# Optimization experiments

Hardware: AMD Instinct MI355X
Metric: run time of the kernel (lower is better)

Reference implementation:

```python
import jax, jax.numpy as jnp
import numpy as np

SCALE = 1.0  # module scale
# dropout is treated as identity (eval mode / deterministic reference)

def setup_inputs() -> dict:
    key = jax.random.key(0)
    k_x, k_w, k1, k2, k3 = jax.random.split(key, 5)
    B, S, D = 4, 4096, 1280
    x = jax.random.normal(k_x, (B, S, D), dtype=jnp.float32)
    W = jax.random.normal(k_w, (D, D), dtype=jnp.float32) * 0.02  # linear.weight [out, in]
    # kron factors are initialized to identity in the module; perturb slightly
    # so the rotation is non-trivial for correctness testing.
    kron_1 = jnp.eye(4, dtype=jnp.float32) + 0.01 * jax.random.normal(k1, (4, 4), dtype=jnp.float32)
    kron_2 = jnp.eye(8, dtype=jnp.float32) + 0.01 * jax.random.normal(k2, (8, 8), dtype=jnp.float32)
    kron_3 = jnp.eye(40, dtype=jnp.float32) + 0.01 * jax.random.normal(k3, (40, 40), dtype=jnp.float32)
    return {"x": x, "W": W, "kron_1": kron_1, "kron_2": kron_2, "kron_3": kron_3}

def reference(x, W, kron_1, kron_2, kron_3):
    # rotate_matrix = kron(kron(k1, k2), k3)  -> [in, in] = [1280, 1280]
    R = jnp.kron(jnp.kron(kron_1, kron_2), kron_3)
    # rotated_weight = (R @ W^T)^T ; F.linear(x, rotated_weight) = x @ (R @ W^T)
    rotated_weight = (R @ W.T).T  # [out, in]
    out = jnp.einsum('bsd,od->bso', x, rotated_weight)
    return out * SCALE
```

## Files before the change

kernel.cpp:

```cpp
#include <hip/hip_runtime.h>
#include <hip/hip_bf16.h>
#include <stdint.h>

typedef __bf16 bf16x8 __attribute__((ext_vector_type(8)));
typedef float floatx4 __attribute__((ext_vector_type(4)));

__device__ __forceinline__ void async_copy16(void* lds, const void* g) {
    __builtin_amdgcn_global_load_lds(
        (const __attribute__((address_space(1))) unsigned int*)g,
        (__attribute__((address_space(3))) unsigned int*)lds,
        16, 0, 0);
}

__global__ __launch_bounds__(256)
void prep(const float* __restrict__ x,
          const float* __restrict__ W,
          const float* __restrict__ K1,
          const float* __restrict__ K2,
          const float* __restrict__ K3,
          __hip_bfloat16* __restrict__ x_bf,
          __hip_bfloat16* __restrict__ Wrot,
          int nConv) {
    const int tid = threadIdx.x;

    if ((int)blockIdx.x < nConv) {
        const size_t i = ((size_t)blockIdx.x * 256 + tid) * 8;
        const float4 a = *(const float4*)(x + i);
        const float4 b = *(const float4*)(x + i + 4);
        bf16x8 v;
        v[0] = (__bf16)a.x; v[1] = (__bf16)a.y; v[2] = (__bf16)a.z; v[3] = (__bf16)a.w;
        v[4] = (__bf16)b.x; v[5] = (__bf16)b.y; v[6] = (__bf16)b.z; v[7] = (__bf16)b.w;
        *(bf16x8*)((__bf16*)x_bf + i) = v;
        return;
    }

    const int o = blockIdx.x - nConv;
    __shared__ __align__(16) float w0[1280];
    __shared__ __align__(16) float t1[1280];
    __shared__ __align__(16) float k3s[1600];
    __shared__ float k2s[64];
    __shared__ float k1s[16];

    for (int i = tid; i < 1280; i += 256) w0[i] = W[o * 1280 + i];
    for (int i = tid; i < 1600; i += 256) k3s[i] = K3[i];
    if (tid < 64) k2s[tid] = K2[tid];
    if (tid < 16) k1s[tid] = K1[tid];
    __syncthreads();

    for (int i = tid; i < 1280; i += 256) {
        const int p = i / 40, d3 = i % 40;
        const float4* w4 = (const float4*)(w0 + p * 40);
        const float4* k4 = (const float4*)(k3s + d3 * 40);
        float acc = 0.f;
#pragma unroll
        for (int t = 0; t < 10; ++t) {
            const float4 a = w4[t], b = k4[t];
            acc += a.x * b.x + a.y * b.y + a.z * b.z + a.w * b.w;
        }
        t1[i] = acc;
    }
    __syncthreads();

    for (int i = tid; i < 1280; i += 256) {
        const int d3 = i % 40, pd = i / 40;
        const int k1 = pd >> 3, d2 = pd & 7;
        float acc = 0.f;
#pragma unroll
        for (int k2 = 0; k2 < 8; ++k2) acc += t1[(k1 * 8 + k2) * 40 + d3] * k2s[d2 * 8 + k2];
        w0[i] = acc;
    }
    __syncthreads();

    for (int i = tid; i < 1280; i += 256) {
        const int d3 = i % 40, pd = i / 40;
        const int d1 = pd >> 3, d2 = pd & 7;
        float acc = 0.f;
#pragma unroll
        for (int k1 = 0; k1 < 4; ++k1) acc += w0[(k1 * 8 + d2) * 40 + d3] * k1s[d1 * 4 + k1];
        Wrot[(size_t)o * 1280 + i] = __float2bfloat16(acc);
    }
}

#define BM 128
#define BN 128
#define BK 64

__global__ __launch_bounds__(256)
void gemm_bt(const __hip_bfloat16* __restrict__ A,
             const __hip_bfloat16* __restrict__ B,
             float* __restrict__ C,
             int M, int N, int K) {
    __shared__ bf16x8 As[1024];
    __shared__ bf16x8 Bs[1024];

    const int tid  = threadIdx.x;
    const int wave = tid >> 6;
    const int lane = tid & 63;
    const int q    = lane >> 4;
    const int r16  = lane & 15;

    const int nTilesN = N / BN;
    const int bn = blockIdx.x % nTilesN;
    const int bm = blockIdx.x / nTilesN;
    const int tileM = bm * BM, tileN = bn * BN;
    const int wm = wave >> 1, wn = wave & 1;

    floatx4 acc[4][4];
#pragma unroll
    for (int i = 0; i < 4; ++i)
#pragma unroll
        for (int j = 0; j < 4; ++j) acc[i][j] = (floatx4){0.f, 0.f, 0.f, 0.f};

    for (int kt = 0; kt < K; kt += BK) {
#pragma unroll
        for (int t = 0; t < 4; ++t) {
            const int g  = wave * 256 + t * 64 + lane;
            const int m  = g >> 3;
            const int sl = g & 7;
            const int kv = sl ^ (m & 7);
            async_copy16(&As[wave * 256 + t * 64],
                         A + (size_t)(tileM + m) * K + kt + kv * 8);
            async_copy16(&Bs[wave * 256 + t * 64],
                         B + (size_t)(tileN + m) * K + kt + kv * 8);
        }
        __syncthreads();

#pragma unroll
        for (int s = 0; s < 2; ++s) {
            bf16x8 af[4], bfr[4];
            const int kv = s * 4 + q;
#pragma unroll
            for (int i = 0; i < 4; ++i) {
                const int m = wm * 64 + i * 16 + r16;
                af[i] = As[m * 8 + (kv ^ (m & 7))];
                const int n = wn * 64 + i * 16 + r16;
                bfr[i] = Bs[n * 8 + (kv ^ (n & 7))];
            }
#pragma unroll
            for (int i = 0; i < 4; ++i)
#pragma unroll
                for (int j = 0; j < 4; ++j)
                    acc[i][j] = __builtin_amdgcn_mfma_f32_16x16x32_bf16(
                        af[i], bfr[j], acc[i][j], 0, 0, 0);
        }
        __syncthreads();
    }

#pragma unroll
    for (int i = 0; i < 4; ++i) {
#pragma unroll
        for (int j = 0; j < 4; ++j) {
            const int col = tileN + wn * 64 + j * 16 + r16;
#pragma unroll
            for (int r = 0; r < 4; ++r) {
                const int row = tileM + wm * 64 + i * 16 + q * 4 + r;
                C[(size_t)row * N + col] = acc[i][j][r];
            }
        }
    }
}

extern "C" void kernel_launch(void* const* d_in, const int* in_sizes, int n_in,
                              void* d_out, int out_size, void* d_ws, size_t ws_size,
                              hipStream_t stream) {
    const float* x  = (const float*)d_in[0];
    const float* W  = (const float*)d_in[1];
    const float* K1 = (const float*)d_in[2];
    const float* K2 = (const float*)d_in[3];
    const float* K3 = (const float*)d_in[4];
    float* out = (float*)d_out;

    const int D = 1280;
    const int M = in_sizes[0] / D;
    const int N = D, K = D;

    __hip_bfloat16* x_bf = (__hip_bfloat16*)d_ws;
    __hip_bfloat16* Wrot = x_bf + (size_t)M * K;

    const int nConv = (M * K) / (256 * 8);
    prep<<<nConv + D, 256, 0, stream>>>(x, W, K1, K2, K3, x_bf, Wrot, nConv);
    gemm_bt<<<(M / BM) * (N / BN), 256, 0, stream>>>(x_bf, Wrot, out, M, N, K);
}
```

Measured before the change: 251.4 us.

## Fuse fp32-to-bf16 conversion of x into GEMM A-tile loading with register prefetch

Removes the separate pass that converted x to bf16 in workspace. The GEMM now loads fp32 A tiles directly into registers, converts them to bf16 and stores them into swizzled LDS. The next tile is prefetched into registers while MFMAs run, and the loop's trailing barrier moves to the start of the next iteration. This saves a full write and read of the bf16 activation copy, but each block now reads fp32 A, doubling the bytes per redundant tile read across column blocks and adding register pressure.

```diff
diff --git a/kernel.cpp b/kernel.cpp
--- a/kernel.cpp
+++ b/kernel.cpp
@@ -13,33 +13,18 @@
 }
 
 __global__ __launch_bounds__(256)
-void prep(const float* __restrict__ x,
-          const float* __restrict__ W,
-          const float* __restrict__ K1,
-          const float* __restrict__ K2,
-          const float* __restrict__ K3,
-          __hip_bfloat16* __restrict__ x_bf,
-          __hip_bfloat16* __restrict__ Wrot,
-          int nConv) {
-    const int tid = threadIdx.x;
-
-    if ((int)blockIdx.x < nConv) {
-        const size_t i = ((size_t)blockIdx.x * 256 + tid) * 8;
-        const float4 a = *(const float4*)(x + i);
-        const float4 b = *(const float4*)(x + i + 4);
-        bf16x8 v;
-        v[0] = (__bf16)a.x; v[1] = (__bf16)a.y; v[2] = (__bf16)a.z; v[3] = (__bf16)a.w;
-        v[4] = (__bf16)b.x; v[5] = (__bf16)b.y; v[6] = (__bf16)b.z; v[7] = (__bf16)b.w;
-        *(bf16x8*)((__bf16*)x_bf + i) = v;
-        return;
-    }
-
-    const int o = blockIdx.x - nConv;
+void kron_rotate_w(const float* __restrict__ W,
+                   const float* __restrict__ K1,
+                   const float* __restrict__ K2,
+                   const float* __restrict__ K3,
+                   __hip_bfloat16* __restrict__ Wrot) {
     __shared__ __align__(16) float w0[1280];
     __shared__ __align__(16) float t1[1280];
     __shared__ __align__(16) float k3s[1600];
     __shared__ float k2s[64];
     __shared__ float k1s[16];
+    const int o   = blockIdx.x;
+    const int tid = threadIdx.x;
 
     for (int i = tid; i < 1280; i += 256) w0[i] = W[o * 1280 + i];
     for (int i = tid; i < 1600; i += 256) k3s[i] = K3[i];
@@ -86,7 +71,7 @@
 #define BK 64
 
 __global__ __launch_bounds__(256)
-void gemm_bt(const __hip_bfloat16* __restrict__ A,
+void gemm_bt(const float* __restrict__ A,
              const __hip_bfloat16* __restrict__ B,
              float* __restrict__ C,
              int M, int N, int K) {
@@ -111,19 +96,52 @@
 #pragma unroll
         for (int j = 0; j < 4; ++j) acc[i][j] = (floatx4){0.f, 0.f, 0.f, 0.f};
 
+    int amrow[4], akv[4];
+#pragma unroll
+    for (int t = 0; t < 4; ++t) {
+        const int g = wave * 256 + t * 64 + lane;
+        amrow[t] = g >> 3;
+        akv[t]   = (g & 7) ^ (amrow[t] & 7);
+    }
+
+    float4 apre[4][2];
+#pragma unroll
+    for (int t = 0; t < 4; ++t) {
+        const float* ga = A + (size_t)(tileM + amrow[t]) * K + akv[t] * 8;
+        apre[t][0] = *(const float4*)ga;
+        apre[t][1] = *(const float4*)(ga + 4);
+    }
+
     for (int kt = 0; kt < K; kt += BK) {
+        __syncthreads();
+
+#pragma unroll
+        for (int t = 0; t < 4; ++t) {
+            bf16x8 v;
+            v[0] = (__bf16)apre[t][0].x; v[1] = (__bf16)apre[t][0].y;
+            v[2] = (__bf16)apre[t][0].z; v[3] = (__bf16)apre[t][0].w;
+            v[4] = (__bf16)apre[t][1].x; v[5] = (__bf16)apre[t][1].y;
+            v[6] = (__bf16)apre[t][1].z; v[7] = (__bf16)apre[t][1].w;
+            As[wave * 256 + t * 64 + lane] = v;
+        }
 #pragma unroll
         for (int t = 0; t < 4; ++t) {
             const int g  = wave * 256 + t * 64 + lane;
             const int m  = g >> 3;
-            const int sl = g & 7;
-            const int kv = sl ^ (m & 7);
-            async_copy16(&As[wave * 256 + t * 64],
-                         A + (size_t)(tileM + m) * K + kt + kv * 8);
+            const int kv = (g & 7) ^ (m & 7);
             async_copy16(&Bs[wave * 256 + t * 64],
                          B + (size_t)(tileN + m) * K + kt + kv * 8);
         }
         __syncthreads();
+
+        if (kt + BK < K) {
+#pragma unroll
+            for (int t = 0; t < 4; ++t) {
+                const float* ga = A + (size_t)(tileM + amrow[t]) * K + (kt + BK) + akv[t] * 8;
+                apre[t][0] = *(const float4*)ga;
+                apre[t][1] = *(const float4*)(ga + 4);
+            }
+        }
 
 #pragma unroll
         for (int s = 0; s < 2; ++s) {
@@ -143,7 +161,6 @@
                     acc[i][j] = __builtin_amdgcn_mfma_f32_16x16x32_bf16(
                         af[i], bfr[j], acc[i][j], 0, 0, 0);
         }
-        __syncthreads();
     }
 
 #pragma unroll
@@ -174,10 +191,8 @@
     const int M = in_sizes[0] / D;
     const int N = D, K = D;
 
-    __hip_bfloat16* x_bf = (__hip_bfloat16*)d_ws;
-    __hip_bfloat16* Wrot = x_bf + (size_t)M * K;
+    __hip_bfloat16* Wrot = (__hip_bfloat16*)d_ws;
 
-    const int nConv = (M * K) / (256 * 8);
-    prep<<<nConv + D, 256, 0, stream>>>(x, W, K1, K2, K3, x_bf, Wrot, nConv);
-    gemm_bt<<<(M / BM) * (N / BN), 256, 0, stream>>>(x_bf, Wrot, out, M, N, K);
+    kron_rotate_w<<<D, 256, 0, stream>>>(W, K1, K2, K3, Wrot);
+    gemm_bt<<<(M / BM) * (N / BN), 256, 0, stream>>>(x, Wrot, out, M, N, K);
 }
```

Result: no change. 255.4 us (+1.6%).
